# Kernel optimization log

Hardware: AMD Instinct MI355X
Metric: run time of the kernel (lower is better)

## Reference

```python
import jax, jax.numpy as jnp
import numpy as np

N = 50000   # nodes per graph
F = 128     # num_features (== hidden width 128 in GCNConv stack)
G = 3       # number_graphs
E = 600000  # edges per graph


def setup_inputs() -> dict:
    key = jax.random.key(0)
    ks = jax.random.split(key, 16)
    s = 0.05  # glorot-ish scale for 128-wide layers
    inp = {
        "x": jax.random.normal(ks[0], (G, N, F), jnp.float32),
        "fc1_w": jax.random.normal(ks[1], (G, F, F), jnp.float32) * s,
        "fc1_b": jnp.zeros((G, F), jnp.float32),
        "w_conv1": jax.random.normal(ks[2], (F, 128), jnp.float32) * s,
        "b_conv1": jnp.zeros((128,), jnp.float32),
        "w_conv2": jax.random.normal(ks[3], (128, 128), jnp.float32) * s,
        "b_conv2": jnp.zeros((128,), jnp.float32),
        "w_dconv1": jax.random.normal(ks[4], (128, 128), jnp.float32) * s,
        "b_dconv1": jnp.zeros((128,), jnp.float32),
        "w_dconv2": jax.random.normal(ks[5], (128, F), jnp.float32) * s,
        "b_dconv2": jnp.zeros((F,), jnp.float32),
        "fc2_w": jax.random.normal(ks[6], (2 * F, F), jnp.float32) * s,
        "fc2_b": jnp.zeros((F,), jnp.float32),
        "att_w": jax.random.normal(ks[7], (G, 128, 128), jnp.float32) * s,
        "edge_index": jax.random.randint(ks[8], (G, 2, E), 0, N, jnp.int64),
    }
    return inp


def _gcn(x, src, dst, W, b):
    # PyG GCNConv: add self-loops, symmetric D^-1/2 (A+I) D^-1/2 normalization
    n = x.shape[0]
    h = x @ W                                  # [N, out]
    loops = jnp.arange(n)
    s = jnp.concatenate([src, loops])
    d = jnp.concatenate([dst, loops])
    deg = jax.ops.segment_sum(jnp.ones_like(d, dtype=h.dtype), d, num_segments=n)
    dinv = jnp.where(deg > 0, jax.lax.rsqrt(deg), 0.0)
    norm = dinv[s] * dinv[d]                   # [E+N]
    out = jax.ops.segment_sum(h[s] * norm[:, None], d, num_segments=n)
    return out + b


_gcn_g = jax.vmap(_gcn, in_axes=(0, 0, 0, None, None))  # over graphs (shared weights)


def _fro(a):
    # Frobenius norm over last two axes (matches torch.norm(., p=2) on a matrix)
    return jnp.sqrt(jnp.sum(a * a, axis=(-2, -1)))


def reference(x, fc1_w, fc1_b, w_conv1, b_conv1, w_conv2, b_conv2,
              w_dconv1, b_dconv1, w_dconv2, b_dconv2, fc2_w, fc2_b,
              att_w, edge_index):
    g = x.shape[0]
    src, dst = edge_index[:, 0], edge_index[:, 1]

    # per-graph fc1 (distinct weights per graph)
    pre_feat = jnp.einsum('gnf,gfo->gno', x, fc1_w) + fc1_b[:, None, :]
    conv1_f = _gcn_g(pre_feat, src, dst, w_conv1, b_conv1)   # [G,N,128]
    enc = _gcn_g(conv1_f, src, dst, w_conv2, b_conv2)        # encoder_H [G,N,128]

    global_vec = jax.nn.sigmoid(jnp.mean(enc, axis=1))       # [G,128]

    # leave-one-out decoder input: (sum_j enc_j - enc_i) / (G-1)
    dec_in = (jnp.sum(enc, axis=0)[None] - enc) / (g - 1)

    own1 = _gcn_g(enc, src, dst, w_dconv1, b_dconv1)         # decov1_f
    own2 = _gcn_g(own1, src, dst, w_dconv2, b_dconv2)        # reconstructed x
    oth1 = _gcn_g(dec_in, src, dst, w_dconv1, b_dconv1)
    oth2 = _gcn_g(oth1, src, dst, w_dconv2, b_dconv2)

    fuse_h = jnp.concatenate([own2, oth2], axis=-1)          # [G,N,2F]
    each_fin = jnp.einsum('gnf,fo->gno', fuse_h, fc2_w) + fc2_b  # [G,N,F]

    # cross-graph attention: sigmoid(H_j @ W_i @ g_i) for all (i, j)
    u = jnp.einsum('ide,ie->id', att_w, global_vec)          # W_i @ g_i -> [G,128]
    S = jax.nn.sigmoid(jnp.einsum('jnd,id->ijn', enc, u))    # [i,j,n]
    L = jnp.transpose(S, (0, 2, 1))                          # [i,n,j]
    L = L / jnp.sum(L, axis=-1, keepdims=True)               # row-normalize over j
    comp_re = jnp.transpose(L, (1, 0, 2)).reshape(x.shape[1], g * g)  # [N, G*G]

    fuse_feat = jax.nn.sigmoid(jnp.mean(each_fin, axis=0))   # [N,F]
    used_feat = jax.nn.elu(jnp.mean(enc, axis=0))            # [N,128]

    obf1 = jnp.sum((_fro(pre_feat - own2) + _fro(conv1_f - own1)) / 2)
    obf0 = jnp.float32(0.0)
    for i in range(g):
        for j in range(g):
            if i != j:
                obf0 = obf0 + _fro(each_fin[i] - each_fin[j])
    return (fuse_feat, used_feat, comp_re, obf1, obf0)
```

## Files before the change

kernel.cpp:

```cpp
#include <hip/hip_runtime.h>

#define NN 50000
#define NFEAT 128
#define NG 3
#define NE 600000

typedef unsigned int u32;
typedef unsigned short u16;
typedef __bf16 bf16x8 __attribute__((ext_vector_type(8)));
typedef float f32x4 __attribute__((ext_vector_type(4)));

__device__ __forceinline__ u16 f2bf(float f){
  u32 u = __float_as_uint(f);
  return (u16)((u + 0x7fffu + ((u >> 16) & 1u)) >> 16);
}
__device__ __forceinline__ float bf2f(u32 s){
  return __uint_as_float((s & 0xffffu) << 16);
}
__device__ __forceinline__ u32 pack2(float a, float b){
  return (u32)f2bf(a) | ((u32)f2bf(b) << 16);
}
__device__ __forceinline__ float sigm(float x){ return 1.f / (1.f + __expf(-x)); }

__global__ void wprep_kernel(const float* fc1w, const float* wc1, const float* wc2,
                             const float* wd1, const float* wd2, const float* fc2w,
                             u16* WT){
  int idx = blockIdx.x * 256 + threadIdx.x;
  if (idx >= 147456) return;
  float v;
  if (idx < 49152){
    int g = idx / 16384, r = idx % 16384; int o = r / 128, f = r % 128;
    v = fc1w[g * 16384 + f * 128 + o];
  } else if (idx < 114688){
    int m = (idx - 49152) / 16384, r = (idx - 49152) % 16384;
    int o = r / 128, f = r % 128;
    const float* w = (m == 0) ? wc1 : (m == 1) ? wc2 : (m == 2) ? wd1 : wd2;
    v = w[f * 128 + o];
  } else {
    int r = idx - 114688; int half = r / 16384; r %= 16384;
    int o = r / 128, f = r % 128;
    v = fc2w[(half * 128 + f) * 128 + o];
  }
  WT[idx] = f2bf(v);
}

__global__ void deg_kernel(const int* ei, int* deg){
  int t = blockIdx.x * 256 + threadIdx.x;
  if (t >= NG * NE) return;
  int g = t / NE, e = t - g * NE;
  int dst = ei[(size_t)g * 2 * NE + NE + e];
  atomicAdd(deg + (size_t)g * NN + dst, 1);
}

__global__ __launch_bounds__(1024) void scan_kernel(const int* deg, int* rowptr, float* dinv){
  const int g = blockIdx.x;
  const int* d = deg + (size_t)g * NN;
  int* rp = rowptr + g * (NN + 1);
  float* di = dinv + (size_t)g * NN;
  __shared__ int s[1024];
  __shared__ int carry;
  if (threadIdx.x == 0) carry = 0;
  __syncthreads();
  for (int base = 0; base <= NN; base += 1024){
    int idx = base + threadIdx.x;
    int v = (idx < NN) ? d[idx] : 0;
    if (idx < NN) di[idx] = rsqrtf((float)(v + 1));
    s[threadIdx.x] = v;
    __syncthreads();
    for (int off = 1; off < 1024; off <<= 1){
      int x = (threadIdx.x >= off) ? s[threadIdx.x - off] : 0;
      __syncthreads();
      s[threadIdx.x] += x;
      __syncthreads();
    }
    int incl = s[threadIdx.x];
    int run = carry;
    if (idx <= NN) rp[idx] = run + incl - v;
    __syncthreads();
    if (threadIdx.x == 1023) carry = run + s[1023];
    __syncthreads();
  }
}

__global__ void fill_kernel(const int* ei, const int* rowptr, int* cursor, int* colbuf){
  int t = blockIdx.x * 256 + threadIdx.x;
  if (t >= NG * NE) return;
  int g = t / NE, e = t - g * NE;
  int src = ei[(size_t)g * 2 * NE + e];
  int dst = ei[(size_t)g * 2 * NE + NE + e];
  int pos = atomicAdd(cursor + (size_t)g * NN + dst, 1);
  colbuf[(size_t)g * NE + rowptr[g * (NN + 1) + dst] + pos] = src;
}

template<int MODE>
__global__ __launch_bounds__(256, 2) void gemm_kernel(
    const void* Ap, const void* Ap2, const u16* W, const u16* W2,
    const float* bias, u16* Out, const float* scale,
    int wPerG, int biasPerG, int hasBias)
{
  __shared__ __align__(16) unsigned char sA[128 * 256];
  __shared__ __align__(16) unsigned char sW[128 * 256];
  const int tid = threadIdx.x;
  const int g = blockIdx.y;
  const int nb = blockIdx.x * 128;
  const int lane = tid & 63, wv = tid >> 6;
  const int wm = (wv & 1) * 64, wn = (wv >> 1) * 64;
  const int l15 = lane & 15, lh = lane >> 4;
  f32x4 acc[4][4] = {};
  constexpr int passes = (MODE == 3) ? 2 : 1;
  for (int p = 0; p < passes; p++){
    if (p) __syncthreads();
    {
      const u16* wsrc = (p ? W2 : W) + (wPerG ? g * 16384 : 0);
      const uint4* w4 = (const uint4*)wsrc;
      for (int i = tid; i < 2048; i += 256){
        int r = i >> 4, c = i & 15;
        uint4 v = w4[i];
        *(uint4*)(sW + r * 256 + ((c * 16) ^ ((r & 7) << 4))) = v;
      }
    }
    if (MODE == 1){
      const float* xp = (const float*)Ap + (size_t)g * NN * NFEAT;
      for (int i = tid; i < 2048; i += 256){
        int r = i >> 4, c = i & 15; int node = nb + r;
        uint4 o = {0, 0, 0, 0};
        if (node < NN){
          const float* row = xp + (size_t)node * NFEAT + c * 8;
          float4 a4 = *(const float4*)row;
          float4 b4 = *(const float4*)(row + 4);
          o.x = pack2(a4.x, a4.y); o.y = pack2(a4.z, a4.w);
          o.z = pack2(b4.x, b4.y); o.w = pack2(b4.z, b4.w);
        }
        *(uint4*)(sA + r * 256 + ((c * 16) ^ ((r & 7) << 4))) = o;
      }
    } else if (MODE == 2){
      const uint4* pe = (const uint4*)((const u16*)Ap + (size_t)g * NN * NFEAT);
      const uint4* ps = (const uint4*)Ap2;
      for (int i = tid; i < 2048; i += 256){
        int r = i >> 4, c = i & 15; int node = nb + r;
        uint4 o = {0, 0, 0, 0};
        if (node < NN){
          uint4 va = pe[(size_t)node * 16 + c];
          uint4 vb = ps[(size_t)node * 16 + c];
          o.x = pack2(0.5f * (bf2f(vb.x) - bf2f(va.x)), 0.5f * (bf2f(vb.x >> 16) - bf2f(va.x >> 16)));
          o.y = pack2(0.5f * (bf2f(vb.y) - bf2f(va.y)), 0.5f * (bf2f(vb.y >> 16) - bf2f(va.y >> 16)));
          o.z = pack2(0.5f * (bf2f(vb.z) - bf2f(va.z)), 0.5f * (bf2f(vb.z >> 16) - bf2f(va.z >> 16)));
          o.w = pack2(0.5f * (bf2f(vb.w) - bf2f(va.w)), 0.5f * (bf2f(vb.w >> 16) - bf2f(va.w >> 16)));
        }
        *(uint4*)(sA + r * 256 + ((c * 16) ^ ((r & 7) << 4))) = o;
      }
    } else {
      const u16* asrc = (const u16*)(p ? Ap2 : Ap) + (size_t)g * NN * NFEAT;
      const uint4* a4 = (const uint4*)asrc;
      for (int i = tid; i < 2048; i += 256){
        int r = i >> 4, c = i & 15; int node = nb + r;
        uint4 v = {0, 0, 0, 0};
        if (node < NN) v = a4[(size_t)node * 16 + c];
        *(uint4*)(sA + r * 256 + ((c * 16) ^ ((r & 7) << 4))) = v;
      }
    }
    __syncthreads();
    #pragma unroll
    for (int k0 = 0; k0 < 128; k0 += 32){
      const int kb = 2 * (k0 + lh * 8);
      bf16x8 af[4], bfr[4];
      #pragma unroll
      for (int t = 0; t < 4; t++){
        int rm = wm + t * 16 + l15;
        af[t] = *reinterpret_cast<const bf16x8*>(sW + rm * 256 + (kb ^ ((rm & 7) << 4)));
        int rn = wn + t * 16 + l15;
        bfr[t] = *reinterpret_cast<const bf16x8*>(sA + rn * 256 + (kb ^ ((rn & 7) << 4)));
      }
      #pragma unroll
      for (int mi = 0; mi < 4; mi++)
        #pragma unroll
        for (int ni = 0; ni < 4; ni++)
          acc[mi][ni] = __builtin_amdgcn_mfma_f32_16x16x32_bf16(af[mi], bfr[ni], acc[mi][ni], 0, 0, 0);
    }
  }
  float scn[4] = {1.f, 1.f, 1.f, 1.f};
  if (scale){
    const float* sg = scale + (size_t)g * NN;
    #pragma unroll
    for (int ni = 0; ni < 4; ni++){
      int node = nb + wn + ni * 16 + l15;
      scn[ni] = (node < NN) ? sg[node] : 0.f;
    }
  }
  u16* outg = Out + (size_t)g * NN * NFEAT;
  #pragma unroll
  for (int mi = 0; mi < 4; mi++){
    int mbase = wm + mi * 16 + lh * 4;
    f32x4 bv = {};
    if (hasBias) bv = *reinterpret_cast<const f32x4*>(bias + (biasPerG ? g * NFEAT : 0) + mbase);
    #pragma unroll
    for (int ni = 0; ni < 4; ni++){
      int node = nb + wn + ni * 16 + l15;
      if (node < NN){
        f32x4 v = acc[mi][ni];
        float s = scn[ni];
        ushort4 o;
        o.x = f2bf((v.x + bv.x) * s); o.y = f2bf((v.y + bv.y) * s);
        o.z = f2bf((v.z + bv.z) * s); o.w = f2bf((v.w + bv.w) * s);
        *reinterpret_cast<ushort4*>(outg + (size_t)node * NFEAT + mbase) = o;
      }
    }
  }
}

template<bool SQ>
__global__ __launch_bounds__(256) void agg_kernel(
    const u16* H, u16* Outp, const float* bias, const float* dinv,
    const int* rowptr, const int* colidx, const u16* Ref, float* sqslot)
{
  const int g = blockIdx.y;
  const int v = blockIdx.x * 4 + (threadIdx.x >> 6);
  const int l = threadIdx.x & 63;
  const int q = l >> 4, sub = l & 15;
  const uint4* h4 = (const uint4*)(H + (size_t)g * NN * NFEAT);
  const int* rp = rowptr + g * (NN + 1);
  const int* ci = colidx + (size_t)g * NE;
  const int e0 = rp[v];
  const int nslot = rp[v + 1] - e0 + 1;
  float a0=0,a1=0,a2=0,a3=0,a4=0,a5=0,a6=0,a7=0;
  const int nIter = (nslot + 7) >> 3;
  for (int it = 0; it < nIter; ++it){
    int sA = it * 8 + q;
    int sB = sA + 4;
    int srcA = (sA == 0) ? v : ((sA < nslot) ? ci[e0 + sA - 1] : v);
    int srcB = (sB < nslot) ? ci[e0 + sB - 1] : v;
    uint4 hA = h4[(size_t)srcA * 16 + sub];
    uint4 hB = h4[(size_t)srcB * 16 + sub];
    if (sA < nslot){
      a0 += bf2f(hA.x); a1 += bf2f(hA.x >> 16);
      a2 += bf2f(hA.y); a3 += bf2f(hA.y >> 16);
      a4 += bf2f(hA.z); a5 += bf2f(hA.z >> 16);
      a6 += bf2f(hA.w); a7 += bf2f(hA.w >> 16);
    }
    if (sB < nslot){
      a0 += bf2f(hB.x); a1 += bf2f(hB.x >> 16);
      a2 += bf2f(hB.y); a3 += bf2f(hB.y >> 16);
      a4 += bf2f(hB.z); a5 += bf2f(hB.z >> 16);
      a6 += bf2f(hB.w); a7 += bf2f(hB.w >> 16);
    }
  }
  a0 += __shfl_xor(a0, 16); a1 += __shfl_xor(a1, 16);
  a2 += __shfl_xor(a2, 16); a3 += __shfl_xor(a3, 16);
  a4 += __shfl_xor(a4, 16); a5 += __shfl_xor(a5, 16);
  a6 += __shfl_xor(a6, 16); a7 += __shfl_xor(a7, 16);
  a0 += __shfl_xor(a0, 32); a1 += __shfl_xor(a1, 32);
  a2 += __shfl_xor(a2, 32); a3 += __shfl_xor(a3, 32);
  a4 += __shfl_xor(a4, 32); a5 += __shfl_xor(a5, 32);
  a6 += __shfl_xor(a6, 32); a7 += __shfl_xor(a7, 32);
  const float dvv = dinv[(size_t)g * NN + v];
  const float4 b4a = *(const float4*)(bias + sub * 8);
  const float4 b4b = *(const float4*)(bias + sub * 8 + 4);
  a0 = a0 * dvv + b4a.x; a1 = a1 * dvv + b4a.y;
  a2 = a2 * dvv + b4a.z; a3 = a3 * dvv + b4a.w;
  a4 = a4 * dvv + b4b.x; a5 = a5 * dvv + b4b.y;
  a6 = a6 * dvv + b4b.z; a7 = a7 * dvv + b4b.w;
  float sq = 0.f;
  if (q == 0){
    uint4 o;
    o.x = pack2(a0, a1); o.y = pack2(a2, a3);
    o.z = pack2(a4, a5); o.w = pack2(a6, a7);
    ((uint4*)(Outp + (size_t)g * NN * NFEAT))[(size_t)v * 16 + sub] = o;
    if (SQ){
      uint4 rv = ((const uint4*)(Ref + (size_t)g * NN * NFEAT))[(size_t)v * 16 + sub];
      float d;
      d = bf2f(rv.x) - a0; sq += d * d; d = bf2f(rv.x >> 16) - a1; sq += d * d;
      d = bf2f(rv.y) - a2; sq += d * d; d = bf2f(rv.y >> 16) - a3; sq += d * d;
      d = bf2f(rv.z) - a4; sq += d * d; d = bf2f(rv.z >> 16) - a5; sq += d * d;
      d = bf2f(rv.w) - a6; sq += d * d; d = bf2f(rv.w >> 16) - a7; sq += d * d;
    }
  }
  if (SQ){
    __shared__ float red[4];
    sq += __shfl_xor(sq, 1); sq += __shfl_xor(sq, 2);
    sq += __shfl_xor(sq, 4); sq += __shfl_xor(sq, 8);
    if (l == 0) red[threadIdx.x >> 6] = sq;
    __syncthreads();
    if (threadIdx.x == 0)
      atomicAdd(sqslot + g, red[0] + red[1] + red[2] + red[3]);
  }
}

__global__ __launch_bounds__(256) void encsum_kernel(
    const u16* Enc, u16* EncSum, float* outUsed, float* colsum)
{
  const int fp = threadIdx.x & 63, sub = threadIdx.x >> 6;
  const u32* e0 = (const u32*)Enc;
  const u32* e1 = e0 + (size_t)NN * 64;
  const u32* e2 = e1 + (size_t)NN * 64;
  u32* es = (u32*)EncSum;
  float cs[6] = {0, 0, 0, 0, 0, 0};
  for (int v = blockIdx.x * 4 + sub; v < NN; v += gridDim.x * 4){
    size_t idx = (size_t)v * 64 + fp;
    u32 a = e0[idx], b = e1[idx], c = e2[idx];
    float axv = bf2f(a), ayv = bf2f(a >> 16);
    float bxv = bf2f(b), byv = bf2f(b >> 16);
    float cxv = bf2f(c), cyv = bf2f(c >> 16);
    cs[0] += axv; cs[1] += ayv; cs[2] += bxv; cs[3] += byv; cs[4] += cxv; cs[5] += cyv;
    float sx = axv + bxv + cxv, sy = ayv + byv + cyv;
    es[idx] = pack2(sx, sy);
    float ux = sx * (1.f / 3.f), uy = sy * (1.f / 3.f);
    float2 o;
    o.x = ux > 0.f ? ux : expm1f(ux);
    o.y = uy > 0.f ? uy : expm1f(uy);
    *(float2*)(outUsed + (size_t)v * NFEAT + 2 * fp) = o;
  }
  __shared__ float red[256];
  #pragma unroll
  for (int q = 0; q < 6; q++){
    red[threadIdx.x] = cs[q];
    __syncthreads();
    if (sub == 0){
      float s = red[fp] + red[64 + fp] + red[128 + fp] + red[192 + fp];
      atomicAdd(&colsum[(q >> 1) * NFEAT + 2 * fp + (q & 1)], s);
    }
    __syncthreads();
  }
}

__global__ void gvecu_kernel(const float* colsum, const float* att, float* u){
  __shared__ float gv[3 * 128];
  const int t = threadIdx.x;
  for (int g = 0; g < 3; g++) gv[g * 128 + t] = sigm(colsum[g * 128 + t] * (1.f / 50000.f));
  __syncthreads();
  for (int i = 0; i < 3; i++){
    float s = 0.f;
    for (int e = 0; e < 128; e++)
      s += att[(size_t)i * 16384 + (size_t)t * 128 + e] * gv[i * 128 + e];
    u[i * 128 + t] = s;
  }
}

__global__ __launch_bounds__(256) void fuse_kernel(const u16* EF, float* outFuse, float* slots){
  const int fp = threadIdx.x & 63, sub = threadIdx.x >> 6;
  const u32* e0 = (const u32*)EF;
  const u32* e1 = e0 + (size_t)NN * 64;
  const u32* e2 = e1 + (size_t)NN * 64;
  float s01 = 0, s02 = 0, s12 = 0;
  for (int v = blockIdx.x * 4 + sub; v < NN; v += gridDim.x * 4){
    size_t idx = (size_t)v * 64 + fp;
    u32 a = e0[idx], b = e1[idx], c = e2[idx];
    float axv = bf2f(a), ayv = bf2f(a >> 16), bxv = bf2f(b), byv = bf2f(b >> 16);
    float cxv = bf2f(c), cyv = bf2f(c >> 16);
    float2 o;
    o.x = sigm((axv + bxv + cxv) * (1.f / 3.f));
    o.y = sigm((ayv + byv + cyv) * (1.f / 3.f));
    *(float2*)(outFuse + (size_t)v * NFEAT + 2 * fp) = o;
    float dx, dy;
    dx = axv - bxv; dy = ayv - byv; s01 += dx * dx + dy * dy;
    dx = axv - cxv; dy = ayv - cyv; s02 += dx * dx + dy * dy;
    dx = bxv - cxv; dy = byv - cyv; s12 += dx * dx + dy * dy;
  }
  __shared__ float red[256];
  float vals[3] = {s01, s02, s12};
  #pragma unroll
  for (int q = 0; q < 3; q++){
    red[threadIdx.x] = vals[q];
    __syncthreads();
    for (int s2 = 128; s2 > 0; s2 >>= 1){
      if (threadIdx.x < s2) red[threadIdx.x] += red[threadIdx.x + s2];
      __syncthreads();
    }
    if (threadIdx.x == 0) atomicAdd(slots + 6 + q, red[0]);
    __syncthreads();
  }
}

__global__ __launch_bounds__(256) void comp_kernel(const u16* Enc, const float* u, float* outC){
  __shared__ float su[384];
  for (int i = threadIdx.x; i < 384; i += 256) su[i] = u[i];
  __syncthreads();
  const int v = blockIdx.x * 4 + (threadIdx.x >> 6);
  const int l = threadIdx.x & 63;
  const u32* e = (const u32*)Enc;
  float ex[3], ey[3];
  #pragma unroll
  for (int j = 0; j < 3; j++){
    u32 t = e[((size_t)j * NN + v) * 64 + l];
    ex[j] = bf2f(t); ey[j] = bf2f(t >> 16);
  }
  float p[9];
  #pragma unroll
  for (int i = 0; i < 3; i++){
    float uxi = su[i * 128 + 2 * l], uyi = su[i * 128 + 2 * l + 1];
    #pragma unroll
    for (int j = 0; j < 3; j++)
      p[i * 3 + j] = ex[j] * uxi + ey[j] * uyi;
  }
  #pragma unroll
  for (int q = 0; q < 9; q++){
    float s = p[q];
    #pragma unroll
    for (int off = 1; off < 64; off <<= 1) s += __shfl_xor(s, off, 64);
    p[q] = s;
  }
  if (l < 9){
    float sg[9];
    #pragma unroll
    for (int q = 0; q < 9; q++) sg[q] = sigm(p[q]);
    float d0 = sg[0] + sg[1] + sg[2], d1 = sg[3] + sg[4] + sg[5], d2 = sg[6] + sg[7] + sg[8];
    float num = sg[0];
    if (l == 1) num = sg[1]; if (l == 2) num = sg[2]; if (l == 3) num = sg[3];
    if (l == 4) num = sg[4]; if (l == 5) num = sg[5]; if (l == 6) num = sg[6];
    if (l == 7) num = sg[7]; if (l == 8) num = sg[8];
    float den = (l < 3) ? d0 : (l < 6) ? d1 : d2;
    outC[(size_t)v * 9 + l] = num / den;
  }
}

__global__ void final_kernel(const float* slots, float* out){
  if (threadIdx.x == 0){
    float obf1 = 0.f;
    for (int g = 0; g < 3; g++)
      obf1 += 0.5f * (sqrtf(slots[3 + g]) + sqrtf(slots[g]));
    float obf0 = 2.f * (sqrtf(slots[6]) + sqrtf(slots[7]) + sqrtf(slots[8]));
    out[13250000] = obf1;
    out[13250001] = obf0;
  }
}

extern "C" void kernel_launch(void* const* d_in, const int* in_sizes, int n_in,
                              void* d_out, int out_size, void* d_ws, size_t ws_size,
                              hipStream_t stream)
{
  (void)in_sizes; (void)n_in; (void)out_size;
  const float* x    = (const float*)d_in[0];
  const float* fc1w = (const float*)d_in[1];
  const float* fc1b = (const float*)d_in[2];
  const float* wc1  = (const float*)d_in[3];
  const float* bc1  = (const float*)d_in[4];
  const float* wc2  = (const float*)d_in[5];
  const float* bc2  = (const float*)d_in[6];
  const float* wd1  = (const float*)d_in[7];
  const float* bd1  = (const float*)d_in[8];
  const float* wd2  = (const float*)d_in[9];
  const float* bd2  = (const float*)d_in[10];
  const float* fc2w = (const float*)d_in[11];
  const float* fc2b = (const float*)d_in[12];
  const float* attw = (const float*)d_in[13];
  const int*   ei   = (const int*)d_in[14];
  float* out = (float*)d_out;
  char* ws = (char*)d_ws;

  constexpr size_t BUFB = (size_t)NG * NN * NFEAT * 2;
  u16* WT   = (u16*)(ws + 0);
  u16* buf0 = (u16*)(ws + 327680);
  u16* buf1 = (u16*)(ws + 327680 + 1 * BUFB);
  u16* buf2 = (u16*)(ws + 327680 + 2 * BUFB);
  u16* buf3 = (u16*)(ws + 327680 + 3 * BUFB);
  u16* buf4 = (u16*)(ws + 327680 + 4 * BUFB);
  u16* buf5 = (u16*)(ws + 327680 + 5 * BUFB);
  size_t off = 327680 + 6 * BUFB;
  u16* encsum = (u16*)(ws + off); off += (size_t)NN * NFEAT * 2;
  float* dinv = (float*)(ws + off); off += (size_t)NG * NN * 4;
  int* rowptr = (int*)(ws + off); off += 600064;
  int* colbuf = (int*)(ws + off); off += (size_t)NG * NE * 4;
  size_t zero_off = off;
  int* deg     = (int*)(ws + off); off += (size_t)NG * NN * 4;
  int* cursor  = (int*)(ws + off); off += (size_t)NG * NN * 4;
  float* colsum = (float*)(ws + off); off += 1536;
  float* slots  = (float*)(ws + off); off += 64;
  size_t zero_bytes = off - zero_off;
  float* uvec = (float*)(ws + off); off += 1536;
  if (ws_size < off) return;

  hipMemsetAsync(ws + zero_off, 0, zero_bytes, stream);

  wprep_kernel<<<576, 256, 0, stream>>>(fc1w, wc1, wc2, wd1, wd2, fc2w, WT);
  deg_kernel<<<7032, 256, 0, stream>>>(ei, deg);
  scan_kernel<<<NG, 1024, 0, stream>>>(deg, rowptr, dinv);
  fill_kernel<<<7032, 256, 0, stream>>>(ei, rowptr, cursor, colbuf);

  const u16* WT_fc1 = WT;
  const u16* WT_c1  = WT + 49152;
  const u16* WT_c2  = WT + 65536;
  const u16* WT_d1  = WT + 81920;
  const u16* WT_d2  = WT + 98304;
  const u16* WT_f2a = WT + 114688;
  const u16* WT_f2b = WT + 131072;
  dim3 gg(391, NG), ag(12500, NG);

  gemm_kernel<1><<<gg, 256, 0, stream>>>(x, nullptr, WT_fc1, nullptr, fc1b, buf0, nullptr, 1, 1, 1);
  gemm_kernel<0><<<gg, 256, 0, stream>>>(buf0, nullptr, WT_c1, nullptr, nullptr, buf3, dinv, 0, 0, 0);
  agg_kernel<false><<<ag, 256, 0, stream>>>(buf3, buf1, bc1, dinv, rowptr, colbuf, nullptr, nullptr);
  gemm_kernel<0><<<gg, 256, 0, stream>>>(buf1, nullptr, WT_c2, nullptr, nullptr, buf3, dinv, 0, 0, 0);
  agg_kernel<false><<<ag, 256, 0, stream>>>(buf3, buf2, bc2, dinv, rowptr, colbuf, nullptr, nullptr);
  encsum_kernel<<<256, 256, 0, stream>>>(buf2, encsum, out + 6400000, colsum);
  gvecu_kernel<<<1, 128, 0, stream>>>(colsum, attw, uvec);
  gemm_kernel<0><<<gg, 256, 0, stream>>>(buf2, nullptr, WT_d1, nullptr, nullptr, buf3, dinv, 0, 0, 0);
  agg_kernel<true><<<ag, 256, 0, stream>>>(buf3, buf4, bd1, dinv, rowptr, colbuf, buf1, slots + 0);
  gemm_kernel<0><<<gg, 256, 0, stream>>>(buf4, nullptr, WT_d2, nullptr, nullptr, buf3, dinv, 0, 0, 0);
  agg_kernel<true><<<ag, 256, 0, stream>>>(buf3, buf5, bd2, dinv, rowptr, colbuf, buf0, slots + 3);
  gemm_kernel<2><<<gg, 256, 0, stream>>>(buf2, encsum, WT_d1, nullptr, nullptr, buf3, dinv, 0, 0, 0);
  agg_kernel<false><<<ag, 256, 0, stream>>>(buf3, buf1, bd1, dinv, rowptr, colbuf, nullptr, nullptr);
  gemm_kernel<0><<<gg, 256, 0, stream>>>(buf1, nullptr, WT_d2, nullptr, nullptr, buf3, dinv, 0, 0, 0);
  agg_kernel<false><<<ag, 256, 0, stream>>>(buf3, buf4, bd2, dinv, rowptr, colbuf, nullptr, nullptr);
  gemm_kernel<3><<<gg, 256, 0, stream>>>(buf5, buf4, WT_f2a, WT_f2b, fc2b, buf0, nullptr, 0, 0, 1);
  fuse_kernel<<<256, 256, 0, stream>>>(buf0, out, slots);
  comp_kernel<<<12500, 256, 0, stream>>>(buf2, uvec, out + 12800000);
  final_kernel<<<1, 64, 0, stream>>>(slots, out);
}
```

Measured before the change: 2.078 ms.

## Fuse decoder own/other GCN aggregations into one interleaved 256-wide pass

The decoder GEMMs now write the own-path and other-path features side by side into one 256-wide buffer. A new agg2 kernel aggregates both halves in a single edge traversal, so the CSR index reads and launches are shared. By linearity, the other path's input 0.5*(encsum-enc) is replaced by a GEMM on encsum shared across graphs; the difference and 0.5 scale are applied after aggregation. This removes the per-graph elementwise prep mode and two aggregation launches. It changes bf16 rounding order and doubles per-node gather width.

```diff
diff --git a/kernel.cpp b/kernel.cpp
--- a/kernel.cpp
+++ b/kernel.cpp
@@ -96,7 +96,7 @@
 __global__ __launch_bounds__(256, 2) void gemm_kernel(
     const void* Ap, const void* Ap2, const u16* W, const u16* W2,
     const float* bias, u16* Out, const float* scale,
-    int wPerG, int biasPerG, int hasBias)
+    int wPerG, int biasPerG, int hasBias, int outStride16, int outOff16, int aPerG)
 {
   __shared__ __align__(16) unsigned char sA[128 * 256];
   __shared__ __align__(16) unsigned char sW[128 * 256];
@@ -133,24 +133,8 @@
         }
         *(uint4*)(sA + r * 256 + ((c * 16) ^ ((r & 7) << 4))) = o;
       }
-    } else if (MODE == 2){
-      const uint4* pe = (const uint4*)((const u16*)Ap + (size_t)g * NN * NFEAT);
-      const uint4* ps = (const uint4*)Ap2;
-      for (int i = tid; i < 2048; i += 256){
-        int r = i >> 4, c = i & 15; int node = nb + r;
-        uint4 o = {0, 0, 0, 0};
-        if (node < NN){
-          uint4 va = pe[(size_t)node * 16 + c];
-          uint4 vb = ps[(size_t)node * 16 + c];
-          o.x = pack2(0.5f * (bf2f(vb.x) - bf2f(va.x)), 0.5f * (bf2f(vb.x >> 16) - bf2f(va.x >> 16)));
-          o.y = pack2(0.5f * (bf2f(vb.y) - bf2f(va.y)), 0.5f * (bf2f(vb.y >> 16) - bf2f(va.y >> 16)));
-          o.z = pack2(0.5f * (bf2f(vb.z) - bf2f(va.z)), 0.5f * (bf2f(vb.z >> 16) - bf2f(va.z >> 16)));
-          o.w = pack2(0.5f * (bf2f(vb.w) - bf2f(va.w)), 0.5f * (bf2f(vb.w >> 16) - bf2f(va.w >> 16)));
-        }
-        *(uint4*)(sA + r * 256 + ((c * 16) ^ ((r & 7) << 4))) = o;
-      }
     } else {
-      const u16* asrc = (const u16*)(p ? Ap2 : Ap) + (size_t)g * NN * NFEAT;
+      const u16* asrc = (const u16*)(p ? Ap2 : Ap) + (aPerG ? (size_t)g * NN * NFEAT : 0);
       const uint4* a4 = (const uint4*)asrc;
       for (int i = tid; i < 2048; i += 256){
         int r = i >> 4, c = i & 15; int node = nb + r;
@@ -187,7 +171,7 @@
       scn[ni] = (node < NN) ? sg[node] : 0.f;
     }
   }
-  u16* outg = Out + (size_t)g * NN * NFEAT;
+  u16* outg = Out + (size_t)g * NN * outStride16;
   #pragma unroll
   for (int mi = 0; mi < 4; mi++){
     int mbase = wm + mi * 16 + lh * 4;
@@ -202,16 +186,15 @@
         ushort4 o;
         o.x = f2bf((v.x + bv.x) * s); o.y = f2bf((v.y + bv.y) * s);
         o.z = f2bf((v.z + bv.z) * s); o.w = f2bf((v.w + bv.w) * s);
-        *reinterpret_cast<ushort4*>(outg + (size_t)node * NFEAT + mbase) = o;
+        *reinterpret_cast<ushort4*>(outg + (size_t)node * outStride16 + outOff16 + mbase) = o;
       }
     }
   }
 }
 
-template<bool SQ>
 __global__ __launch_bounds__(256) void agg_kernel(
     const u16* H, u16* Outp, const float* bias, const float* dinv,
-    const int* rowptr, const int* colidx, const u16* Ref, float* sqslot)
+    const int* rowptr, const int* colidx)
 {
   const int g = blockIdx.y;
   const int v = blockIdx.x * 4 + (threadIdx.x >> 6);
@@ -222,7 +205,7 @@
   const int* ci = colidx + (size_t)g * NE;
   const int e0 = rp[v];
   const int nslot = rp[v + 1] - e0 + 1;
-  float a0=0,a1=0,a2=0,a3=0,a4=0,a5=0,a6=0,a7=0;
+  float aa[8] = {0,0,0,0,0,0,0,0};
   const int nIter = (nslot + 7) >> 3;
   for (int it = 0; it < nIter; ++it){
     int sA = it * 8 + q;
@@ -232,47 +215,117 @@
     uint4 hA = h4[(size_t)srcA * 16 + sub];
     uint4 hB = h4[(size_t)srcB * 16 + sub];
     if (sA < nslot){
-      a0 += bf2f(hA.x); a1 += bf2f(hA.x >> 16);
-      a2 += bf2f(hA.y); a3 += bf2f(hA.y >> 16);
-      a4 += bf2f(hA.z); a5 += bf2f(hA.z >> 16);
-      a6 += bf2f(hA.w); a7 += bf2f(hA.w >> 16);
+      aa[0] += bf2f(hA.x); aa[1] += bf2f(hA.x >> 16);
+      aa[2] += bf2f(hA.y); aa[3] += bf2f(hA.y >> 16);
+      aa[4] += bf2f(hA.z); aa[5] += bf2f(hA.z >> 16);
+      aa[6] += bf2f(hA.w); aa[7] += bf2f(hA.w >> 16);
     }
     if (sB < nslot){
-      a0 += bf2f(hB.x); a1 += bf2f(hB.x >> 16);
-      a2 += bf2f(hB.y); a3 += bf2f(hB.y >> 16);
-      a4 += bf2f(hB.z); a5 += bf2f(hB.z >> 16);
-      a6 += bf2f(hB.w); a7 += bf2f(hB.w >> 16);
-    }
-  }
-  a0 += __shfl_xor(a0, 16); a1 += __shfl_xor(a1, 16);
-  a2 += __shfl_xor(a2, 16); a3 += __shfl_xor(a3, 16);
-  a4 += __shfl_xor(a4, 16); a5 += __shfl_xor(a5, 16);
-  a6 += __shfl_xor(a6, 16); a7 += __shfl_xor(a7, 16);
-  a0 += __shfl_xor(a0, 32); a1 += __shfl_xor(a1, 32);
-  a2 += __shfl_xor(a2, 32); a3 += __shfl_xor(a3, 32);
-  a4 += __shfl_xor(a4, 32); a5 += __shfl_xor(a5, 32);
-  a6 += __shfl_xor(a6, 32); a7 += __shfl_xor(a7, 32);
+      aa[0] += bf2f(hB.x); aa[1] += bf2f(hB.x >> 16);
+      aa[2] += bf2f(hB.y); aa[3] += bf2f(hB.y >> 16);
+      aa[4] += bf2f(hB.z); aa[5] += bf2f(hB.z >> 16);
+      aa[6] += bf2f(hB.w); aa[7] += bf2f(hB.w >> 16);
+    }
+  }
+  #pragma unroll
+  for (int i = 0; i < 8; i++){
+    aa[i] += __shfl_xor(aa[i], 16);
+    aa[i] += __shfl_xor(aa[i], 32);
+  }
+  if (q == 0){
+    const float dvv = dinv[(size_t)g * NN + v];
+    const float4 b4a = *(const float4*)(bias + sub * 8);
+    const float4 b4b = *(const float4*)(bias + sub * 8 + 4);
+    uint4 o;
+    o.x = pack2(aa[0] * dvv + b4a.x, aa[1] * dvv + b4a.y);
+    o.y = pack2(aa[2] * dvv + b4a.z, aa[3] * dvv + b4a.w);
+    o.z = pack2(aa[4] * dvv + b4b.x, aa[5] * dvv + b4b.y);
+    o.w = pack2(aa[6] * dvv + b4b.z, aa[7] * dvv + b4b.w);
+    ((uint4*)(Outp + (size_t)g * NN * NFEAT))[(size_t)v * 16 + sub] = o;
+  }
+}
+
+template<int COMB, bool SQ>
+__global__ __launch_bounds__(256) void agg2_kernel(
+    const u16* F, u16* OutOwn, u16* OutOth, const float* bias, const float* dinv,
+    const int* rowptr, const int* colidx, const u16* Ref, float* sqslot)
+{
+  const int g = blockIdx.y;
+  const int v = blockIdx.x * 4 + (threadIdx.x >> 6);
+  const int l = threadIdx.x & 63;
+  const int q = l >> 4, sub = l & 15;
+  const uint4* h4 = (const uint4*)(F + (size_t)g * NN * 256);
+  const int* rp = rowptr + g * (NN + 1);
+  const int* ci = colidx + (size_t)g * NE;
+  const int e0 = rp[v];
+  const int nslot = rp[v + 1] - e0 + 1;
+  float uu[8] = {0,0,0,0,0,0,0,0};
+  float tt[8] = {0,0,0,0,0,0,0,0};
+  const int nIter = (nslot + 7) >> 3;
+  for (int it = 0; it < nIter; ++it){
+    int sA = it * 8 + q;
+    int sB = sA + 4;
+    int srcA = (sA == 0) ? v : ((sA < nslot) ? ci[e0 + sA - 1] : v);
+    int srcB = (sB < nslot) ? ci[e0 + sB - 1] : v;
+    uint4 uA = h4[(size_t)srcA * 32 + sub];
+    uint4 tA = h4[(size_t)srcA * 32 + 16 + sub];
+    uint4 uB = h4[(size_t)srcB * 32 + sub];
+    uint4 tB = h4[(size_t)srcB * 32 + 16 + sub];
+    if (sA < nslot){
+      uu[0] += bf2f(uA.x); uu[1] += bf2f(uA.x >> 16);
+      uu[2] += bf2f(uA.y); uu[3] += bf2f(uA.y >> 16);
+      uu[4] += bf2f(uA.z); uu[5] += bf2f(uA.z >> 16);
+      uu[6] += bf2f(uA.w); uu[7] += bf2f(uA.w >> 16);
+      tt[0] += bf2f(tA.x); tt[1] += bf2f(tA.x >> 16);
+      tt[2] += bf2f(tA.y); tt[3] += bf2f(tA.y >> 16);
+      tt[4] += bf2f(tA.z); tt[5] += bf2f(tA.z >> 16);
+      tt[6] += bf2f(tA.w); tt[7] += bf2f(tA.w >> 16);
+    }
+    if (sB < nslot){
+      uu[0] += bf2f(uB.x); uu[1] += bf2f(uB.x >> 16);
+      uu[2] += bf2f(uB.y); uu[3] += bf2f(uB.y >> 16);
+      uu[4] += bf2f(uB.z); uu[5] += bf2f(uB.z >> 16);
+      uu[6] += bf2f(uB.w); uu[7] += bf2f(uB.w >> 16);
+      tt[0] += bf2f(tB.x); tt[1] += bf2f(tB.x >> 16);
+      tt[2] += bf2f(tB.y); tt[3] += bf2f(tB.y >> 16);
+      tt[4] += bf2f(tB.z); tt[5] += bf2f(tB.z >> 16);
+      tt[6] += bf2f(tB.w); tt[7] += bf2f(tB.w >> 16);
+    }
+  }
+  #pragma unroll
+  for (int i = 0; i < 8; i++){
+    uu[i] += __shfl_xor(uu[i], 16); uu[i] += __shfl_xor(uu[i], 32);
+    tt[i] += __shfl_xor(tt[i], 16); tt[i] += __shfl_xor(tt[i], 32);
+  }
   const float dvv = dinv[(size_t)g * NN + v];
   const float4 b4a = *(const float4*)(bias + sub * 8);
   const float4 b4b = *(const float4*)(bias + sub * 8 + 4);
-  a0 = a0 * dvv + b4a.x; a1 = a1 * dvv + b4a.y;
-  a2 = a2 * dvv + b4a.z; a3 = a3 * dvv + b4a.w;
-  a4 = a4 * dvv + b4b.x; a5 = a5 * dvv + b4b.y;
-  a6 = a6 * dvv + b4b.z; a7 = a7 * dvv + b4b.w;
+  float own[8], oth[8];
+  const float bb[8] = {b4a.x, b4a.y, b4a.z, b4a.w, b4b.x, b4b.y, b4b.z, b4b.w};
+  #pragma unroll
+  for (int i = 0; i < 8; i++){
+    own[i] = uu[i] * dvv + bb[i];
+    if (COMB) oth[i] = (tt[i] - uu[i]) * dvv * 0.5f + bb[i];
+    else      oth[i] = tt[i] * dvv + bb[i];
+  }
   float sq = 0.f;
   if (q == 0){
-    uint4 o;
-    o.x = pack2(a0, a1); o.y = pack2(a2, a3);
-    o.z = pack2(a4, a5); o.w = pack2(a6, a7);
-    ((uint4*)(Outp + (size_t)g * NN * NFEAT))[(size_t)v * 16 + sub] = o;
     if (SQ){
       uint4 rv = ((const uint4*)(Ref + (size_t)g * NN * NFEAT))[(size_t)v * 16 + sub];
       float d;
-      d = bf2f(rv.x) - a0; sq += d * d; d = bf2f(rv.x >> 16) - a1; sq += d * d;
-      d = bf2f(rv.y) - a2; sq += d * d; d = bf2f(rv.y >> 16) - a3; sq += d * d;
-      d = bf2f(rv.z) - a4; sq += d * d; d = bf2f(rv.z >> 16) - a5; sq += d * d;
-      d = bf2f(rv.w) - a6; sq += d * d; d = bf2f(rv.w >> 16) - a7; sq += d * d;
-    }
+      d = bf2f(rv.x) - own[0]; sq += d * d; d = bf2f(rv.x >> 16) - own[1]; sq += d * d;
+      d = bf2f(rv.y) - own[2]; sq += d * d; d = bf2f(rv.y >> 16) - own[3]; sq += d * d;
+      d = bf2f(rv.z) - own[4]; sq += d * d; d = bf2f(rv.z >> 16) - own[5]; sq += d * d;
+      d = bf2f(rv.w) - own[6]; sq += d * d; d = bf2f(rv.w >> 16) - own[7]; sq += d * d;
+    }
+    uint4 o;
+    o.x = pack2(own[0], own[1]); o.y = pack2(own[2], own[3]);
+    o.z = pack2(own[4], own[5]); o.w = pack2(own[6], own[7]);
+    ((uint4*)(OutOwn + (size_t)g * NN * NFEAT))[(size_t)v * 16 + sub] = o;
+    uint4 o2;
+    o2.x = pack2(oth[0], oth[1]); o2.y = pack2(oth[2], oth[3]);
+    o2.z = pack2(oth[4], oth[5]); o2.w = pack2(oth[6], oth[7]);
+    ((uint4*)(OutOth + (size_t)g * NN * NFEAT))[(size_t)v * 16 + sub] = o2;
   }
   if (SQ){
     __shared__ float red[4];
@@ -451,9 +504,8 @@
   u16* buf0 = (u16*)(ws + 327680);
   u16* buf1 = (u16*)(ws + 327680 + 1 * BUFB);
   u16* buf2 = (u16*)(ws + 327680 + 2 * BUFB);
-  u16* buf3 = (u16*)(ws + 327680 + 3 * BUFB);
-  u16* buf4 = (u16*)(ws + 327680 + 4 * BUFB);
-  u16* buf5 = (u16*)(ws + 327680 + 5 * BUFB);
+  u16* bufT = (u16*)(ws + 327680 + 3 * BUFB);
+  u16* bufF = (u16*)(ws + 327680 + 4 * BUFB);
   size_t off = 327680 + 6 * BUFB;
   u16* encsum = (u16*)(ws + off); off += (size_t)NN * NFEAT * 2;
   float* dinv = (float*)(ws + off); off += (size_t)NG * NN * 4;
@@ -484,23 +536,21 @@
   const u16* WT_f2b = WT + 131072;
   dim3 gg(391, NG), ag(12500, NG);
 
-  gemm_kernel<1><<<gg, 256, 0, stream>>>(x, nullptr, WT_fc1, nullptr, fc1b, buf0, nullptr, 1, 1, 1);
-  gemm_kernel<0><<<gg, 256, 0, stream>>>(buf0, nullptr, WT_c1, nullptr, nullptr, buf3, dinv, 0, 0, 0);
-  agg_kernel<false><<<ag, 256, 0, stream>>>(buf3, buf1, bc1, dinv, rowptr, colbuf, nullptr, nullptr);
-  gemm_kernel<0><<<gg, 256, 0, stream>>>(buf1, nullptr, WT_c2, nullptr, nullptr, buf3, dinv, 0, 0, 0);
-  agg_kernel<false><<<ag, 256, 0, stream>>>(buf3, buf2, bc2, dinv, rowptr, colbuf, nullptr, nullptr);
+  gemm_kernel<1><<<gg, 256, 0, stream>>>(x, nullptr, WT_fc1, nullptr, fc1b, buf0, nullptr, 1, 1, 1, 128, 0, 1);
+  gemm_kernel<0><<<gg, 256, 0, stream>>>(buf0, nullptr, WT_c1, nullptr, nullptr, bufT, dinv, 0, 0, 0, 128, 0, 1);
+  agg_kernel<<<ag, 256, 0, stream>>>(bufT, buf1, bc1, dinv, rowptr, colbuf);
+  gemm_kernel<0><<<gg, 256, 0, stream>>>(buf1, nullptr, WT_c2, nullptr, nullptr, bufT, dinv, 0, 0, 0, 128, 0, 1);
+  agg_kernel<<<ag, 256, 0, stream>>>(bufT, buf2, bc2, dinv, rowptr, colbuf);
   encsum_kernel<<<256, 256, 0, stream>>>(buf2, encsum, out + 6400000, colsum);
   gvecu_kernel<<<1, 128, 0, stream>>>(colsum, attw, uvec);
-  gemm_kernel<0><<<gg, 256, 0, stream>>>(buf2, nullptr, WT_d1, nullptr, nullptr, buf3, dinv, 0, 0, 0);
-  agg_kernel<true><<<ag, 256, 0, stream>>>(buf3, buf4, bd1, dinv, rowptr, colbuf, buf1, slots + 0);
-  gemm_kernel<0><<<gg, 256, 0, stream>>>(buf4, nullptr, WT_d2, nullptr, nullptr, buf3, dinv, 0, 0, 0);
-  agg_kernel<true><<<ag, 256, 0, stream>>>(buf3, buf5, bd2, dinv, rowptr, colbuf, buf0, slots + 3);
-  gemm_kernel<2><<<gg, 256, 0, stream>>>(buf2, encsum, WT_d1, nullptr, nullptr, buf3, dinv, 0, 0, 0);
-  agg_kernel<false><<<ag, 256, 0, stream>>>(buf3, buf1, bd1, dinv, rowptr, colbuf, nullptr, nullptr);
-  gemm_kernel<0><<<gg, 256, 0, stream>>>(buf1, nullptr, WT_d2, nullptr, nullptr, buf3, dinv, 0, 0, 0);
-  agg_kernel<false><<<ag, 256, 0, stream>>>(buf3, buf4, bd2, dinv, rowptr, colbuf, nullptr, nullptr);
-  gemm_kernel<3><<<gg, 256, 0, stream>>>(buf5, buf4, WT_f2a, WT_f2b, fc2b, buf0, nullptr, 0, 0, 1);
-  fuse_kernel<<<256, 256, 0, stream>>>(buf0, out, slots);
+  gemm_kernel<0><<<gg, 256, 0, stream>>>(buf2, nullptr, WT_d1, nullptr, nullptr, bufF, dinv, 0, 0, 0, 256, 0, 1);
+  gemm_kernel<0><<<gg, 256, 0, stream>>>(encsum, nullptr, WT_d1, nullptr, nullptr, bufF, dinv, 0, 0, 0, 256, 128, 0);
+  agg2_kernel<1, true><<<ag, 256, 0, stream>>>(bufF, bufT, buf1, bd1, dinv, rowptr, colbuf, buf1, slots + 0);
+  gemm_kernel<0><<<gg, 256, 0, stream>>>(bufT, nullptr, WT_d2, nullptr, nullptr, bufF, dinv, 0, 0, 0, 256, 0, 1);
+  gemm_kernel<0><<<gg, 256, 0, stream>>>(buf1, nullptr, WT_d2, nullptr, nullptr, bufF, dinv, 0, 0, 0, 256, 128, 1);
+  agg2_kernel<0, true><<<ag, 256, 0, stream>>>(bufF, buf0, buf1, bd2, dinv, rowptr, colbuf, buf0, slots + 3);
+  gemm_kernel<3><<<gg, 256, 0, stream>>>(buf0, buf1, WT_f2a, WT_f2b, fc2b, bufF, nullptr, 0, 0, 1, 128, 0, 1);
+  fuse_kernel<<<256, 256, 0, stream>>>(bufF, out, slots);
   comp_kernel<<<12500, 256, 0, stream>>>(buf2, uvec, out + 12800000);
   final_kernel<<<1, 64, 0, stream>>>(slots, out);
 }
```

Measured after the change: 1.946 ms. 1.07x faster.
